# Performance work log

Measured on AMD Instinct MI355X. Metric: run time of the kernel, lower is better.

Reference implementation:

```python
import jax, jax.numpy as jnp
import numpy as np

N_HEAD = 16
ROPE_BASE = 10000.0


def setup_inputs() -> dict:
    key = jax.random.key(0)
    ks = jax.random.split(key, 5)
    B, T, C = 4, 1024, 2048
    s_in = 1.0 / np.sqrt(C)
    return {
        "x": jax.random.normal(ks[0], (B, T, C), dtype=jnp.float32),
        "w_attn": jax.random.normal(ks[1], (C, 3 * C), dtype=jnp.float32) * s_in,
        "b_attn": jax.random.normal(ks[2], (3 * C,), dtype=jnp.float32) * 0.01,
        "w_proj": jax.random.normal(ks[3], (C, C), dtype=jnp.float32) * s_in,
        "b_proj": jax.random.normal(ks[4], (C,), dtype=jnp.float32) * 0.01,
    }


def _rope(x, cos, sin):
    # x: (B, T, H, D); cos/sin: (T, D//2) -> broadcast over B, H
    d2 = x.shape[-1] // 2
    x1, x2 = x[..., :d2], x[..., d2:]
    c = cos[None, :, None, :]
    s = sin[None, :, None, :]
    return jnp.concatenate([x1 * c - x2 * s, x1 * s + x2 * c], axis=-1)


def reference(x, w_attn, b_attn, w_proj, b_proj):
    B, T, C = x.shape
    H = N_HEAD
    D = C // H
    qkv = (x @ w_attn + b_attn).reshape(B, T, 3, H, D)
    q, k, v = qkv[:, :, 0], qkv[:, :, 1], qkv[:, :, 2]  # (B, T, H, D)

    # Rotary embedding (GPT-NeoX / rotate-half style, full head dim)
    inv_freq = 1.0 / (ROPE_BASE ** (jnp.arange(0, D, 2, dtype=jnp.float32) / D))
    freqs = jnp.arange(T, dtype=jnp.float32)[:, None] * inv_freq[None, :]  # (T, D//2)
    cos, sin = jnp.cos(freqs), jnp.sin(freqs)
    q = _rope(q, cos, sin)
    k = _rope(k, cos, sin)

    scale = 1.0 / jnp.sqrt(jnp.asarray(D, dtype=x.dtype))
    att = jnp.einsum("bqhd,bkhd->bhqk", q, k) * scale  # (B, H, T, T)
    causal = jnp.tril(jnp.ones((T, T), dtype=bool))
    att = jnp.where(causal[None, None], att, jnp.asarray(-jnp.inf, dtype=att.dtype))
    att = jax.nn.softmax(att, axis=-1)
    y = jnp.einsum("bhqk,bkhd->bqhd", att, v).reshape(B, T, C)
    return y @ w_proj + b_proj
```

## Files before the change

kernel.cpp:

```cpp
#include <hip/hip_runtime.h>
#include <math.h>

#define T_SEQ 1024
#define C_DIM 2048
#define H_NUM 16
#define D_HEAD 128
#define BT 4096
#define QKV_N 6144

typedef __bf16 bf16x8 __attribute__((ext_vector_type(8)));
typedef float f32x4 __attribute__((ext_vector_type(4)));
typedef unsigned short u16;
typedef unsigned int u32;

#define AS1C(p) ((const __attribute__((address_space(1))) void*)(p))
#define AS3(p)  ((__attribute__((address_space(3))) void*)(p))

__device__ __forceinline__ u16 f2bf(float f) {
    u32 u = __builtin_bit_cast(u32, f);
    u += 0x7fffu + ((u >> 16) & 1u);
    return (u16)(u >> 16);
}
__device__ __forceinline__ void unpack8(uint4 u, float* f) {
    const u32 w0 = u.x, w1 = u.y, w2 = u.z, w3 = u.w;
    f[0] = __builtin_bit_cast(float, w0 << 16);
    f[1] = __builtin_bit_cast(float, w0 & 0xffff0000u);
    f[2] = __builtin_bit_cast(float, w1 << 16);
    f[3] = __builtin_bit_cast(float, w1 & 0xffff0000u);
    f[4] = __builtin_bit_cast(float, w2 << 16);
    f[5] = __builtin_bit_cast(float, w2 & 0xffff0000u);
    f[6] = __builtin_bit_cast(float, w3 << 16);
    f[7] = __builtin_bit_cast(float, w3 & 0xffff0000u);
}
__device__ __forceinline__ uint4 pack8(const float* f) {
    uint4 u;
    u.x = (u32)f2bf(f[0]) | ((u32)f2bf(f[1]) << 16);
    u.y = (u32)f2bf(f[2]) | ((u32)f2bf(f[3]) << 16);
    u.z = (u32)f2bf(f[4]) | ((u32)f2bf(f[5]) << 16);
    u.w = (u32)f2bf(f[6]) | ((u32)f2bf(f[7]) << 16);
    return u;
}

__device__ __forceinline__ void ph_barrier() {
    asm volatile("" ::: "memory");
    __builtin_amdgcn_s_barrier();
    asm volatile("" ::: "memory");
}

__global__ __launch_bounds__(256) void cast_bf16(
    const float* __restrict__ in, u16* __restrict__ out)
{
    int i = blockIdx.x * 256 + threadIdx.x;
    float4 v = ((const float4*)in)[i];
    ushort4 o;
    o.x = f2bf(v.x); o.y = f2bf(v.y); o.z = f2bf(v.z); o.w = f2bf(v.w);
    ((ushort4*)out)[i] = o;
}

__global__ __launch_bounds__(256) void transpose_cast(
    const float* __restrict__ in, u16* __restrict__ out, int R, int Cc)
{
    __shared__ float tile[32][33];
    const int c0 = blockIdx.x * 32, r0 = blockIdx.y * 32;
    const int tx = threadIdx.x & 31, ty = threadIdx.x >> 5;
#pragma unroll
    for (int i = 0; i < 32; i += 8)
        tile[ty + i][tx] = in[(size_t)(r0 + ty + i) * Cc + c0 + tx];
    __syncthreads();
#pragma unroll
    for (int i = 0; i < 32; i += 8)
        out[(size_t)(c0 + ty + i) * R + r0 + tx] = f2bf(tile[tx][ty + i]);
}

template <int BN, int OUT_BF16>
__global__ __launch_bounds__(512, 4) void gemm_bf16_ov(
    const u16* __restrict__ A,
    const u16* __restrict__ Bt,
    const float* __restrict__ bias,
    void* __restrict__ Cout,
    int M, int N, int K)
{
    constexpr int BI  = BN / 64;
    constexpr int NTW = BN / 64;
    constexpr int WCOLS = BN / 4;
    __shared__ alignas(16) char lds[2][16384 + BN * 128];

    const int tid  = threadIdx.x;
    const int lane = tid & 63;
    const int w    = tid >> 6;
    const int wr   = w >> 2;
    const int wc   = w & 3;
    const int l15  = lane & 15;
    const int l4   = lane >> 4;
    const int m0   = blockIdx.y * 128;
    const int n0   = blockIdx.x * BN;
    const int NT   = K >> 6;

    f32x4 acc[4][NTW] = {};

    const int srow  = w * 16 + (lane >> 3);
    const int sslot = (lane & 7) ^ (lane >> 3);
    const size_t aoff = (size_t)(m0 + srow) * K + sslot * 8;
    const int brow_s = w * 8 + (lane >> 3);
    const size_t boff = (size_t)(n0 + brow_s) * K + sslot * 8;

    auto stageA = [&](char* buf, int k0) {
#pragma unroll
        for (int i = 0; i < 2; ++i)
            __builtin_amdgcn_global_load_lds(
                AS1C(A + aoff + (size_t)(i * 8) * K + k0),
                AS3(buf + w * 2048 + i * 1024), 16, 0, 0);
    };
    auto stageB = [&](char* buf, int k0) {
#pragma unroll
        for (int i = 0; i < BI; ++i)
            __builtin_amdgcn_global_load_lds(
                AS1C(Bt + boff + (size_t)(i * 64) * K + k0),
                AS3(buf + 16384 + i * 8192 + w * 1024), 16, 0, 0);
    };

    stageB(lds[0], 0);
    stageA(lds[0], 0);
    stageB(lds[1], 64);
    if (BI == 3) asm volatile("s_waitcnt vmcnt(3)" ::: "memory");
    else         asm volatile("s_waitcnt vmcnt(2)" ::: "memory");
    ph_barrier();

    const int sl0  = (l4 ^ (l15 & 7)) << 4;
    const int sl1  = sl0 ^ 64;
    const int arow = (wr * 64 + l15) * 128;
    const int brow = 16384 + (wc * WCOLS + l15) * 128;

    for (int kt = 0; kt < NT; ++kt) {
        char* cb = lds[kt & 1];
        char* nb = lds[(kt & 1) ^ 1];

        bf16x8 bfr[NTW][2], af[2][2];
#pragma unroll
        for (int nt = 0; nt < NTW; ++nt) {
            bfr[nt][0] = __builtin_bit_cast(bf16x8,
                *(const uint4*)(cb + brow + nt * 2048 + sl0));
            bfr[nt][1] = __builtin_bit_cast(bf16x8,
                *(const uint4*)(cb + brow + nt * 2048 + sl1));
        }
#pragma unroll
        for (int mt = 0; mt < 2; ++mt) {
            af[mt][0] = __builtin_bit_cast(bf16x8,
                *(const uint4*)(cb + arow + mt * 2048 + sl0));
            af[mt][1] = __builtin_bit_cast(bf16x8,
                *(const uint4*)(cb + arow + mt * 2048 + sl1));
        }
        if (kt + 1 < NT) stageA(nb, (kt + 1) << 6);
        __builtin_amdgcn_s_setprio(1);
#pragma unroll
        for (int mt = 0; mt < 2; ++mt)
#pragma unroll
            for (int nt = 0; nt < NTW; ++nt)
#pragma unroll
                for (int kk = 0; kk < 2; ++kk)
                    acc[mt][nt] = __builtin_amdgcn_mfma_f32_16x16x32_bf16(
                        af[mt][kk], bfr[nt][kk], acc[mt][nt], 0, 0, 0);
        __builtin_amdgcn_s_setprio(0);
        ph_barrier();

        bf16x8 ag[2][2];
#pragma unroll
        for (int mt = 0; mt < 2; ++mt) {
            ag[mt][0] = __builtin_bit_cast(bf16x8,
                *(const uint4*)(cb + arow + (2 + mt) * 2048 + sl0));
            ag[mt][1] = __builtin_bit_cast(bf16x8,
                *(const uint4*)(cb + arow + (2 + mt) * 2048 + sl1));
        }
        if (kt + 2 < NT) stageB(cb, (kt + 2) << 6);
        __builtin_amdgcn_s_setprio(1);
#pragma unroll
        for (int mt = 0; mt < 2; ++mt)
#pragma unroll
            for (int nt = 0; nt < NTW; ++nt)
#pragma unroll
                for (int kk = 0; kk < 2; ++kk)
                    acc[mt + 2][nt] = __builtin_amdgcn_mfma_f32_16x16x32_bf16(
                        ag[mt][kk], bfr[nt][kk], acc[mt + 2][nt], 0, 0, 0);
        __builtin_amdgcn_s_setprio(0);
        if (kt < NT - 2) {
            if (BI == 3) asm volatile("s_waitcnt vmcnt(3)" ::: "memory");
            else         asm volatile("s_waitcnt vmcnt(2)" ::: "memory");
        } else {
            asm volatile("s_waitcnt vmcnt(0)" ::: "memory");
        }
        ph_barrier();
    }

#pragma unroll
    for (int nt = 0; nt < NTW; ++nt) {
        const int colg = n0 + wc * WCOLS + nt * 16 + l15;
        const float bv = bias[colg];
#pragma unroll
        for (int mt = 0; mt < 4; ++mt) {
            const int rowb = m0 + wr * 64 + mt * 16 + l4 * 4;
#pragma unroll
            for (int r = 0; r < 4; ++r) {
                const float v = acc[mt][nt][r] + bv;
                if (OUT_BF16)
                    ((u16*)Cout)[(size_t)(rowb + r) * N + colg] = f2bf(v);
                else
                    ((float*)Cout)[(size_t)(rowb + r) * N + colg] = v;
            }
        }
    }
}

__global__ __launch_bounds__(256) void rope_table(
    float* __restrict__ ct, float* __restrict__ st)
{
    const int i = blockIdx.x * 256 + threadIdx.x;
    const int d2 = i & 63, t = i >> 6;
    const float invf = expf(-(float)d2 * (9.210340371976184f / 64.0f));
    const float fr = (float)t * invf;
    ct[i] = cosf(fr);
    st[i] = sinf(fr);
}

__global__ __launch_bounds__(256) void rope_kv(
    const u16* __restrict__ qkv, const float* __restrict__ ct,
    const float* __restrict__ st,
    u16* __restrict__ Qc, u16* __restrict__ Kc, u16* __restrict__ Vt)
{
    __shared__ u16 vtile[128][264];
    const int tid = threadIdx.x;
    const int blk = blockIdx.x;
    const int tt = blk & 3;
    const int h  = (blk >> 2) & 15;
    const int b  = blk >> 6;
    const int bh = b * 16 + h;

    const int c8 = tid & 15;
    const int rg = tid >> 4;
    const float sgn = (c8 < 8) ? -1.f : 1.f;

#pragma unroll 4
    for (int s = 0; s < 16; ++s) {
        const int row = s * 16 + rg;
        const int t   = tt * 256 + row;
        const size_t rsrc = (size_t)(b * T_SEQ + t) * QKV_N + h * D_HEAD;
        const size_t rdst = (size_t)(bh * T_SEQ + t) * D_HEAD + c8 * 8;

        const float* crow = ct + t * 64 + (c8 & 7) * 8;
        const float* srow = st + t * 64 + (c8 & 7) * 8;
        float cs[8], sn[8];
        *(float4*)(cs)     = *(const float4*)(crow);
        *(float4*)(cs + 4) = *(const float4*)(crow + 4);
        *(float4*)(sn)     = *(const float4*)(srow);
        *(float4*)(sn + 4) = *(const float4*)(srow + 4);

#pragma unroll
        for (int part = 0; part < 2; ++part) {
            uint4 u = *(const uint4*)(qkv + rsrc + part * C_DIM + c8 * 8);
            uint4 pu;
            pu.x = (u32)__shfl_xor((int)u.x, 8, 64);
            pu.y = (u32)__shfl_xor((int)u.y, 8, 64);
            pu.z = (u32)__shfl_xor((int)u.z, 8, 64);
            pu.w = (u32)__shfl_xor((int)u.w, 8, 64);
            float f[8], pf[8], o[8];
            unpack8(u, f); unpack8(pu, pf);
#pragma unroll
            for (int i = 0; i < 8; ++i)
                o[i] = f[i] * cs[i] + sgn * pf[i] * sn[i];
            u16* outp = (part ? Kc : Qc) + rdst;
            *(uint4*)outp = pack8(o);
        }
    }

    const int t = tt * 256 + tid;
    const size_t vsrc = (size_t)(b * T_SEQ + t) * QKV_N + 2 * C_DIM + h * D_HEAD;
#pragma unroll
    for (int c = 0; c < 16; ++c) {
        uint4 v = *(const uint4*)(qkv + vsrc + c * 8);
        u16 e[8];
        e[0] = (u16)(v.x & 0xffff); e[1] = (u16)(v.x >> 16);
        e[2] = (u16)(v.y & 0xffff); e[3] = (u16)(v.y >> 16);
        e[4] = (u16)(v.z & 0xffff); e[5] = (u16)(v.z >> 16);
        e[6] = (u16)(v.w & 0xffff); e[7] = (u16)(v.w >> 16);
#pragma unroll
        for (int j = 0; j < 8; ++j)
            vtile[c * 8 + j][tid] = e[j];
    }
    __syncthreads();

    const int dl = tid >> 5;
    const int jc = (tid & 31) * 8;
    u16* vt = Vt + ((size_t)bh * D_HEAD) * T_SEQ + (size_t)tt * 256;
#pragma unroll
    for (int pass = 0; pass < 16; ++pass) {
        const int d = pass * 8 + dl;
        *(uint4*)(vt + (size_t)d * T_SEQ + jc) = *(const uint4*)&vtile[d][jc];
    }
}

__global__ __launch_bounds__(256) void attn_mfma(
    const u16* __restrict__ Qc,
    const u16* __restrict__ Kc,
    const u16* __restrict__ Vt,
    u16* __restrict__ y)
{
    __shared__ alignas(16) char KsL[2][16384];
    __shared__ alignas(16) char VtsL[2][16384];
    __shared__ alignas(16) char PwL[4][2176];

    const int tid  = threadIdx.x;
    const int lane = tid & 63;
    const int w    = tid >> 6;
    const int l15  = lane & 15;
    const int l4   = lane >> 4;
    const int p    = blockIdx.x;
    const int bh   = blockIdx.y;
    const int h    = bh & 15;
    const int b    = bh >> 4;

    const size_t kbase = (size_t)bh * T_SEQ * D_HEAD;
    const size_t vbase = (size_t)bh * D_HEAD * T_SEQ;
    const float scale = 0.08838834764831845f;
    char* pw = PwL[w];

    for (int half = 0; half < 2; ++half) {
        const int qt = half ? (15 - p) : p;

        const int qrow = qt * 64 + w * 16 + l15;
        const u16* qptr = Qc + ((size_t)(bh * T_SEQ + qrow)) * D_HEAD;
        bf16x8 qf[4];
#pragma unroll
        for (int f = 0; f < 4; ++f)
            qf[f] = __builtin_bit_cast(bf16x8, *(const uint4*)(qptr + f * 32 + l4 * 8));

        f32x4 o[8] = {};
        float lrow[4] = {};

        __syncthreads();

        {
            const u16* ksrc = Kc + kbase + (size_t)(0 * 64 + lane) * D_HEAD;
#pragma unroll
            for (int i = 0; i < 4; ++i) {
                const int cd = w * 4 + i;
                __builtin_amdgcn_global_load_lds(AS1C(ksrc + cd * 8),
                                                 AS3(KsL[0] + cd * 1024), 16, 0, 0);
            }
#pragma unroll
            for (int i = 0; i < 4; ++i) {
                const int jc = w + (i >> 1) * 4;
                const int dh = i & 1;
                const u16* vsrc = Vt + vbase + (size_t)(dh * 64 + lane) * T_SEQ
                                  + 0 * 64 + jc * 8;
                __builtin_amdgcn_global_load_lds(AS1C(vsrc),
                                                 AS3(VtsL[0] + jc * 2048 + dh * 1024), 16, 0, 0);
            }
        }

        int buf = 0;
        for (int kt = 0; kt <= qt; ++kt, buf ^= 1) {
            __syncthreads();
            if (kt < qt) {
                const int kn = kt + 1;
                char* kb = KsL[buf ^ 1];
                char* vb = VtsL[buf ^ 1];
                const u16* ksrc = Kc + kbase + (size_t)(kn * 64 + lane) * D_HEAD;
#pragma unroll
                for (int i = 0; i < 4; ++i) {
                    const int cd = w * 4 + i;
                    __builtin_amdgcn_global_load_lds(AS1C(ksrc + cd * 8),
                                                     AS3(kb + cd * 1024), 16, 0, 0);
                }
#pragma unroll
                for (int i = 0; i < 4; ++i) {
                    const int jc = w + (i >> 1) * 4;
                    const int dh = i & 1;
                    const u16* vsrc = Vt + vbase + (size_t)(dh * 64 + lane) * T_SEQ
                                      + kn * 64 + jc * 8;
                    __builtin_amdgcn_global_load_lds(AS1C(vsrc),
                                                     AS3(vb + jc * 2048 + dh * 1024), 16, 0, 0);
                }
            }

            const char* kbuf = KsL[buf];
            const char* vbuf = VtsL[buf];

            f32x4 sacc[4] = {};
#pragma unroll
            for (int nb = 0; nb < 4; ++nb)
#pragma unroll
                for (int kc = 0; kc < 4; ++kc) {
                    bf16x8 kf = __builtin_bit_cast(bf16x8,
                        *(const uint4*)(kbuf + (kc * 4 + l4) * 1024 + (nb * 16 + l15) * 16));
                    sacc[nb] = __builtin_amdgcn_mfma_f32_16x16x32_bf16(
                        qf[kc], kf, sacc[nb], 0, 0, 0);
                }

#pragma unroll
            for (int nb = 0; nb < 4; ++nb)
#pragma unroll
                for (int r = 0; r < 4; ++r) {
                    const bool masked =
                        (kt == qt) && ((nb * 16 + l15) > (w * 16 + l4 * 4 + r));
                    const float e = masked ? 0.f
                        : __expf(sacc[nb][r] * scale - 8.0f);
                    sacc[nb][r] = e;
                    lrow[r] += e;
                }

#pragma unroll
            for (int nb = 0; nb < 4; ++nb)
#pragma unroll
                for (int r = 0; r < 4; ++r) {
                    const int j = nb * 16 + l15;
                    const int q = l4 * 4 + r;
                    *(u16*)(pw + (j >> 3) * 272 + q * 16 + (j & 7) * 2) =
                        f2bf(sacc[nb][r]);
                }

            bf16x8 pf[2];
#pragma unroll
            for (int kc2 = 0; kc2 < 2; ++kc2)
                pf[kc2] = __builtin_bit_cast(bf16x8,
                    *(const uint4*)(pw + (kc2 * 4 + l4) * 272 + l15 * 16));
#pragma unroll
            for (int db = 0; db < 8; ++db)
#pragma unroll
                for (int kc2 = 0; kc2 < 2; ++kc2) {
                    bf16x8 vf = __builtin_bit_cast(bf16x8,
                        *(const uint4*)(vbuf + (kc2 * 4 + l4) * 2048 + (db * 16 + l15) * 16));
                    o[db] = __builtin_amdgcn_mfma_f32_16x16x32_bf16(
                        pf[kc2], vf, o[db], 0, 0, 0);
                }
        }

        float inv[4];
#pragma unroll
        for (int r = 0; r < 4; ++r) {
            float ls = lrow[r];
#pragma unroll
            for (int off = 1; off < 16; off <<= 1)
                ls += __shfl_xor(ls, off, 64);
            inv[r] = 1.f / ls;
        }
#pragma unroll
        for (int db = 0; db < 8; ++db)
#pragma unroll
            for (int r = 0; r < 4; ++r) {
                const int q = qt * 64 + w * 16 + l4 * 4 + r;
                const int d = h * D_HEAD + db * 16 + l15;
                y[(size_t)(b * T_SEQ + q) * C_DIM + d] = f2bf(o[db][r] * inv[r]);
            }
    }
}

extern "C" void kernel_launch(void* const* d_in, const int* in_sizes, int n_in,
                              void* d_out, int out_size, void* d_ws, size_t ws_size,
                              hipStream_t stream) {
    const float* x      = (const float*)d_in[0];
    const float* w_attn = (const float*)d_in[1];
    const float* b_attn = (const float*)d_in[2];
    const float* w_proj = (const float*)d_in[3];
    const float* b_proj = (const float*)d_in[4];
    float* out = (float*)d_out;

    char* ws = (char*)d_ws;
    u16* xb   = (u16*)(ws);
    u16* waT  = (u16*)(ws + 16777216);
    u16* Qc   = (u16*)(ws);
    u16* Kc   = (u16*)(ws + 16777216);
    u16* Vt   = (u16*)(ws + 33554432);
    u16* qkvb = (u16*)(ws + 50331648);
    u16* wpT  = (u16*)(ws + 50331648);
    u16* yb   = (u16*)(ws + 100663296);
    float* ct = (float*)(ws + 100663296);
    float* st = ct + 65536;

    cast_bf16<<<(BT * C_DIM / 4) / 256, 256, 0, stream>>>(x, xb);
    transpose_cast<<<dim3(QKV_N / 32, C_DIM / 32), 256, 0, stream>>>(w_attn, waT, C_DIM, QKV_N);
    rope_table<<<(T_SEQ * 64) / 256, 256, 0, stream>>>(ct, st);

    gemm_bf16_ov<192, 1><<<dim3(QKV_N / 192, BT / 128), 512, 0, stream>>>(
        xb, waT, b_attn, qkvb, BT, QKV_N, C_DIM);

    rope_kv<<<256, 256, 0, stream>>>(qkvb, ct, st, Qc, Kc, Vt);

    transpose_cast<<<dim3(C_DIM / 32, C_DIM / 32), 256, 0, stream>>>(w_proj, wpT, C_DIM, C_DIM);

    attn_mfma<<<dim3(8, 4 * H_NUM), 256, 0, stream>>>(Qc, Kc, Vt, yb);

    gemm_bf16_ov<128, 0><<<dim3(C_DIM / 128, BT / 128), 512, 0, stream>>>(
        yb, wpT, b_proj, out, BT, C_DIM, C_DIM);
}
```

Before: 351.2 us.

## Add 128x128 K32 bf16 GEMM kernel with split A/B staging for QKV projection

Introduces a new bf16 MFMA GEMM using 128x128 tiles with a K-step of 32 and 16KB double-buffered LDS, and uses it for the QKV projection instead of the 192-wide tile kernel. The smaller LDS footprint and launch bound of 6 aim for higher occupancy, and A and B tile loads are staggered between two half-iterations to overlap global-to-LDS copies with MFMA work. In exchange, the shorter K step means more barriers per unit of work and less reuse per tile. Output stores are scalar per element, which may be less coalesced.

Measured after the change: 375.6 us. 6.9% more time.

```diff
diff --git a/kernel.cpp b/kernel.cpp
--- a/kernel.cpp
+++ b/kernel.cpp
@@ -70,6 +70,111 @@
 #pragma unroll
     for (int i = 0; i < 32; i += 8)
         out[(size_t)(c0 + ty + i) * R + r0 + tx] = f2bf(tile[tx][ty + i]);
+}
+
+template <int OUT_BF16>
+__global__ __launch_bounds__(512, 6) void gemm_bf16_q32(
+    const u16* __restrict__ A,
+    const u16* __restrict__ Bt,
+    const float* __restrict__ bias,
+    void* __restrict__ Cout,
+    int M, int N, int K)
+{
+    __shared__ alignas(16) char lds[2][16384];
+
+    const int tid  = threadIdx.x;
+    const int lane = tid & 63;
+    const int w    = tid >> 6;
+    const int wr   = w >> 2;
+    const int wc   = w & 3;
+    const int l15  = lane & 15;
+    const int l4   = lane >> 4;
+    const int m0   = blockIdx.y * 128;
+    const int n0   = blockIdx.x * 128;
+    const int NT   = K >> 5;
+
+    f32x4 acc[4][2] = {};
+
+    const int srow  = w * 16 + (lane >> 2);
+    const int sslot = (lane & 3) ^ ((lane >> 3) & 3);
+    const size_t aoff = (size_t)(m0 + srow) * K + sslot * 8;
+    const size_t boff = (size_t)(n0 + srow) * K + sslot * 8;
+
+    auto stageA = [&](char* buf, int k0) {
+        __builtin_amdgcn_global_load_lds(AS1C(A + aoff + k0),
+                                         AS3(buf + w * 1024), 16, 0, 0);
+    };
+    auto stageB = [&](char* buf, int k0) {
+        __builtin_amdgcn_global_load_lds(AS1C(Bt + boff + k0),
+                                         AS3(buf + 8192 + w * 1024), 16, 0, 0);
+    };
+
+    stageB(lds[0], 0);
+    stageA(lds[0], 0);
+    stageB(lds[1], 32);
+    asm volatile("s_waitcnt vmcnt(1)" ::: "memory");
+    ph_barrier();
+
+    const int sl   = (l4 ^ ((l15 >> 1) & 3)) << 4;
+    const int arow = (wr * 64 + l15) * 64;
+    const int brow = 8192 + (wc * 32 + l15) * 64;
+
+    for (int kt = 0; kt < NT; ++kt) {
+        char* cb = lds[kt & 1];
+        char* nb = lds[(kt & 1) ^ 1];
+
+        bf16x8 bfr[2], af[2];
+        bfr[0] = __builtin_bit_cast(bf16x8, *(const uint4*)(cb + brow + sl));
+        bfr[1] = __builtin_bit_cast(bf16x8, *(const uint4*)(cb + brow + 1024 + sl));
+        af[0]  = __builtin_bit_cast(bf16x8, *(const uint4*)(cb + arow + sl));
+        af[1]  = __builtin_bit_cast(bf16x8, *(const uint4*)(cb + arow + 1024 + sl));
+        if (kt + 1 < NT) stageA(nb, (kt + 1) << 5);
+        __builtin_amdgcn_s_setprio(1);
+#pragma unroll
+        for (int mt = 0; mt < 2; ++mt)
+#pragma unroll
+            for (int nt = 0; nt < 2; ++nt)
+                acc[mt][nt] = __builtin_amdgcn_mfma_f32_16x16x32_bf16(
+                    af[mt], bfr[nt], acc[mt][nt], 0, 0, 0);
+        __builtin_amdgcn_s_setprio(0);
+        ph_barrier();
+
+        bf16x8 ag[2];
+        ag[0] = __builtin_bit_cast(bf16x8, *(const uint4*)(cb + arow + 2048 + sl));
+        ag[1] = __builtin_bit_cast(bf16x8, *(const uint4*)(cb + arow + 3072 + sl));
+        if (kt + 2 < NT) stageB(cb, (kt + 2) << 5);
+        __builtin_amdgcn_s_setprio(1);
+#pragma unroll
+        for (int mt = 0; mt < 2; ++mt)
+#pragma unroll
+            for (int nt = 0; nt < 2; ++nt)
+                acc[mt + 2][nt] = __builtin_amdgcn_mfma_f32_16x16x32_bf16(
+                    ag[mt], bfr[nt], acc[mt + 2][nt], 0, 0, 0);
+        __builtin_amdgcn_s_setprio(0);
+        if (kt < NT - 2)
+            asm volatile("s_waitcnt vmcnt(1)" ::: "memory");
+        else
+            asm volatile("s_waitcnt vmcnt(0)" ::: "memory");
+        ph_barrier();
+    }
+
+#pragma unroll
+    for (int nt = 0; nt < 2; ++nt) {
+        const int colg = n0 + wc * 32 + nt * 16 + l15;
+        const float bv = bias[colg];
+#pragma unroll
+        for (int mt = 0; mt < 4; ++mt) {
+            const int rowb = m0 + wr * 64 + mt * 16 + l4 * 4;
+#pragma unroll
+            for (int r = 0; r < 4; ++r) {
+                const float v = acc[mt][nt][r] + bv;
+                if (OUT_BF16)
+                    ((u16*)Cout)[(size_t)(rowb + r) * N + colg] = f2bf(v);
+                else
+                    ((float*)Cout)[(size_t)(rowb + r) * N + colg] = v;
+            }
+        }
+    }
 }
 
 template <int BN, int OUT_BF16>
@@ -479,7 +584,7 @@
     transpose_cast<<<dim3(QKV_N / 32, C_DIM / 32), 256, 0, stream>>>(w_attn, waT, C_DIM, QKV_N);
     rope_table<<<(T_SEQ * 64) / 256, 256, 0, stream>>>(ct, st);
 
-    gemm_bf16_ov<192, 1><<<dim3(QKV_N / 192, BT / 128), 512, 0, stream>>>(
+    gemm_bf16_q32<1><<<dim3(QKV_N / 128, BT / 128), 512, 0, stream>>>(
         xb, waT, b_attn, qkvb, BT, QKV_N, C_DIM);
 
     rope_kv<<<256, 256, 0, stream>>>(qkvb, ct, st, Qc, Kc, Vt);
```
